# Kernel tuning notes

Hardware: AMD Instinct MI355X
Metric: run time of the kernel (lower is better)

## Reference

```python
import jax, jax.numpy as jnp
import numpy as np

IMG = 800.0
STRIDES = (4, 8, 16, 32)
SIZES = (32.0, 64.0, 128.0, 256.0)
RATIOS = (0.5, 1.0, 2.0)
A = 3
PRE_NMS_K = 1000
POST_NMS = 512
NMS_TH = 0.7
POOL = 7
_MEAN = np.array([0.485, 0.456, 0.406], np.float32).reshape(3, 1, 1)
_STD = np.array([0.229, 0.224, 0.225], np.float32).reshape(3, 1, 1)


def _conv(x, w, stride=1):
    # x: [C,H,W], w: [O,I,kh,kw]
    return jax.lax.conv_general_dilated(x[None], w, (stride, stride), 'SAME',
                                        dimension_numbers=('NCHW', 'OIHW', 'NCHW'))[0]


def _make_anchors(fh, fw, stride, size):
    cy = (np.arange(fh, dtype=np.float32) + 0.5) * stride
    cx = (np.arange(fw, dtype=np.float32) + 0.5) * stride
    ws = np.array([size / np.sqrt(r) for r in RATIOS], np.float32)
    hs = np.array([size * np.sqrt(r) for r in RATIOS], np.float32)
    gy, gx = np.meshgrid(cy, cx, indexing='ij')
    x1 = gx[..., None] - ws / 2; y1 = gy[..., None] - hs / 2
    x2 = gx[..., None] + ws / 2; y2 = gy[..., None] + hs / 2
    return jnp.asarray(np.stack([x1, y1, x2, y2], -1).reshape(-1, 4))  # [fh*fw*A,4]


def _decode(anchors, deltas):
    aw = anchors[:, 2] - anchors[:, 0]; ah = anchors[:, 3] - anchors[:, 1]
    acx = anchors[:, 0] + aw * 0.5; acy = anchors[:, 1] + ah * 0.5
    dw = jnp.clip(deltas[:, 2], -4.0, 4.0); dh = jnp.clip(deltas[:, 3], -4.0, 4.0)
    cx = acx + deltas[:, 0] * aw; cy = acy + deltas[:, 1] * ah
    w = aw * jnp.exp(dw); h = ah * jnp.exp(dh)
    boxes = jnp.stack([cx - w * 0.5, cy - h * 0.5, cx + w * 0.5, cy + h * 0.5], -1)
    return jnp.clip(boxes, 0.0, IMG)


def _nms(boxes, scores, iou_th, max_out):
    # Greedy NMS with fixed output size (jit-compatible).
    x1, y1, x2, y2 = boxes[:, 0], boxes[:, 1], boxes[:, 2], boxes[:, 3]
    areas = (x2 - x1) * (y2 - y1)

    def body(i, state):
        s, keep = state
        idx = jnp.argmax(s)
        keep = keep.at[i].set(idx)
        ix1 = jnp.maximum(x1, x1[idx]); iy1 = jnp.maximum(y1, y1[idx])
        ix2 = jnp.minimum(x2, x2[idx]); iy2 = jnp.minimum(y2, y2[idx])
        inter = jnp.maximum(ix2 - ix1, 0.0) * jnp.maximum(iy2 - iy1, 0.0)
        iou = inter / (areas + areas[idx] - inter + 1e-6)
        return jnp.where(iou > iou_th, -jnp.inf, s), keep

    _, keep = jax.lax.fori_loop(0, max_out, body, (scores, jnp.zeros(max_out, jnp.int32)))
    return keep


def _roi_align(feat, rois, scale):
    # feat: [C,H,W]; rois: [N,4] in image coords; bilinear, 1 sample per bin.
    C, H, W = feat.shape
    n = rois.shape[0]
    x1 = rois[:, 0] * scale; y1 = rois[:, 1] * scale
    bw = (rois[:, 2] - rois[:, 0]) * scale / POOL
    bh = (rois[:, 3] - rois[:, 1]) * scale / POOL
    j = jnp.arange(POOL, dtype=feat.dtype) + 0.5
    gx = jnp.broadcast_to((x1[:, None] + j * bw[:, None] - 0.5)[:, None, :], (n, POOL, POOL))
    gy = jnp.broadcast_to((y1[:, None] + j * bh[:, None] - 0.5)[:, :, None], (n, POOL, POOL))
    fx = jnp.clip(jnp.floor(gx), 0.0, W - 1); fy = jnp.clip(jnp.floor(gy), 0.0, H - 1)
    x0 = fx.astype(jnp.int32); y0 = fy.astype(jnp.int32)
    x1i = jnp.minimum(x0 + 1, W - 1); y1i = jnp.minimum(y0 + 1, H - 1)
    wx = jnp.clip(gx - fx, 0.0, 1.0); wy = jnp.clip(gy - fy, 0.0, 1.0)
    v = (feat[:, y0, x0] * (1 - wy) * (1 - wx) + feat[:, y0, x1i] * (1 - wy) * wx
         + feat[:, y1i, x0] * wy * (1 - wx) + feat[:, y1i, x1i] * wy * wx)  # [C,N,P,P]
    return jnp.transpose(v, (1, 0, 2, 3))  # [N,C,P,P]


def _forward(x, stem_w, c2_w, c3_w, c4_w, c5_w, fpn2_w, fpn3_w, fpn4_w, fpn5_w,
             rpn_w, rpn_cls_w, rpn_box_w, fc1_w, fc1_b, fc2_w, fc2_b,
             cls_w, cls_b, breg_w, breg_b):
    x = (x - _MEAN) / _STD  # ImageNet normalize
    h = jax.nn.relu(_conv(x, stem_w, 2))      # [64,400,400]
    c2 = jax.nn.relu(_conv(h, c2_w, 2))       # [256,200,200] stride 4
    c3 = jax.nn.relu(_conv(c2, c3_w, 2))      # stride 8
    c4 = jax.nn.relu(_conv(c3, c4_w, 2))      # stride 16
    c5 = jax.nn.relu(_conv(c4, c5_w, 2))      # stride 32
    feats = [_conv(c2, fpn2_w), _conv(c3, fpn3_w), _conv(c4, fpn4_w), _conv(c5, fpn5_w)]

    boxes_l, scores_l = [], []
    for lvl, f in enumerate(feats):
        t = jax.nn.relu(_conv(f, rpn_w))
        fh, fw = f.shape[1], f.shape[2]
        logits = jnp.transpose(_conv(t, rpn_cls_w), (1, 2, 0)).reshape(-1)  # [fh*fw*A]
        deltas = jnp.transpose(_conv(t, rpn_box_w).reshape(A, 4, fh, fw), (2, 3, 0, 1)).reshape(-1, 4)
        anchors = _make_anchors(fh, fw, STRIDES[lvl], SIZES[lvl])
        dec = _decode(anchors, deltas)
        k = min(PRE_NMS_K, logits.shape[0])
        sc, idx = jax.lax.top_k(logits, k)
        boxes_l.append(dec[idx]); scores_l.append(sc)

    boxes = jnp.concatenate(boxes_l, 0)
    scores = jnp.concatenate(scores_l, 0)
    keep = _nms(boxes, scores, NMS_TH, POST_NMS)
    props = boxes[keep]  # [POST_NMS,4]

    pooled = _roi_align(feats[0], props, 1.0 / STRIDES[0])  # [N,256,7,7]
    v = pooled.reshape(POST_NMS, -1)
    v = jax.nn.relu(v @ fc1_w + fc1_b)
    v = jax.nn.relu(v @ fc2_w + fc2_b)
    return v @ cls_w + cls_b, v @ breg_w + breg_b, props, scores[keep]


def setup_inputs() -> dict:
    key = jax.random.key(0)
    ks = jax.random.split(key, 18)

    def he(k, shape):
        fan_in = int(np.prod(shape[1:])) if len(shape) == 4 else shape[0]
        return jax.random.normal(k, shape, jnp.float32) * float(np.sqrt(2.0 / fan_in))

    inp = {'x': jax.random.uniform(ks[0], (3, 800, 800), jnp.float32)}
    inp['stem_w'] = he(ks[1], (64, 3, 7, 7))
    inp['c2_w'] = he(ks[2], (256, 64, 3, 3))
    for i, name in enumerate(['c3_w', 'c4_w', 'c5_w', 'fpn2_w', 'fpn3_w', 'fpn4_w', 'fpn5_w', 'rpn_w']):
        inp[name] = he(ks[3 + i], (256, 256, 3, 3))
    inp['rpn_cls_w'] = he(ks[11], (3, 256, 1, 1))
    inp['rpn_box_w'] = he(ks[12], (12, 256, 1, 1))
    inp['fc1_w'] = he(ks[13], (12544, 1024)); inp['fc1_b'] = jnp.zeros((1024,), jnp.float32)
    inp['fc2_w'] = he(ks[14], (1024, 1024)); inp['fc2_b'] = jnp.zeros((1024,), jnp.float32)
    inp['cls_w'] = he(ks[15], (1024, 2)); inp['cls_b'] = jnp.zeros((2,), jnp.float32)
    inp['breg_w'] = he(ks[16], (1024, 8)); inp['breg_b'] = jnp.zeros((8,), jnp.float32)
    return inp


def reference(x, stem_w, c2_w, c3_w, c4_w, c5_w, fpn2_w, fpn3_w, fpn4_w, fpn5_w,
              rpn_w, rpn_cls_w, rpn_box_w, fc1_w, fc1_b, fc2_w, fc2_b,
              cls_w, cls_b, breg_w, breg_b):
    return _forward(x, stem_w, c2_w, c3_w, c4_w, c5_w, fpn2_w, fpn3_w, fpn4_w, fpn5_w,
                    rpn_w, rpn_cls_w, rpn_box_w, fc1_w, fc1_b, fc2_w, fc2_b,
                    cls_w, cls_b, breg_w, breg_b)
```

## Files before the change

### kernel.cpp

```cpp
#include <hip/hip_runtime.h>
#include <math.h>


#define DI __device__ __forceinline__

typedef short short8 __attribute__((ext_vector_type(8)));
typedef float float16v __attribute__((ext_vector_type(16)));

DI unsigned fkey(float f) {
  unsigned u = __float_as_uint(f);
  return (u & 0x80000000u) ? ~u : (u | 0x80000000u);
}

DI unsigned short f2bf(float f) {
  unsigned u = __float_as_uint(f);
  unsigned r = (u + 0x7FFFu + ((u >> 16) & 1u)) >> 16;
  return (unsigned short)r;
}

__global__ __launch_bounds__(256) void stem_conv(const float* __restrict__ x,
                                                 const float* __restrict__ w,
                                                 float* __restrict__ out) {
  __shared__ float tin[3 * 37 * 37];
  __shared__ float tw[4 * 147];
  const int x0 = blockIdx.x * 16, y0 = blockIdx.y * 16, co0 = blockIdx.z * 4;
  const int tid = threadIdx.x;
  for (int i = tid; i < 4 * 147; i += 256) tw[i] = w[co0 * 147 + i];
  const int ix0 = x0 * 2 - 2, iy0 = y0 * 2 - 2;
  const float mean[3] = {0.485f, 0.456f, 0.406f};
  const float stdv[3] = {0.229f, 0.224f, 0.225f};
  for (int i = tid; i < 3 * 37 * 37; i += 256) {
    int c = i / 1369, r = i % 1369, yy = r / 37, xx = r % 37;
    int gy = iy0 + yy, gx = ix0 + xx;
    float v = 0.f;
    if ((unsigned)gy < 800u && (unsigned)gx < 800u)
      v = __fdiv_rn(__fsub_rn(x[c * 640000 + gy * 800 + gx], mean[c]), stdv[c]);
    tin[i] = v;
  }
  __syncthreads();
  const int tx = tid & 15, ty = tid >> 4;
  float acc[4] = {0.f, 0.f, 0.f, 0.f};
  for (int c = 0; c < 3; ++c)
    for (int ky = 0; ky < 7; ++ky)
#pragma unroll
      for (int kx = 0; kx < 7; ++kx) {
        float v = tin[c * 1369 + (ty * 2 + ky) * 37 + (tx * 2 + kx)];
#pragma unroll
        for (int co = 0; co < 4; ++co)
          acc[co] = fmaf(v, tw[co * 147 + c * 49 + ky * 7 + kx], acc[co]);
      }
  int ox = x0 + tx, oy = y0 + ty;
#pragma unroll
  for (int co = 0; co < 4; ++co)
    out[(size_t)(co0 + co) * 160000 + oy * 400 + ox] = fmaxf(acc[co], 0.f);
}

__global__ void repack_w32(const float* __restrict__ w,
                           float* __restrict__ wpk, int Cin) {
  int i = blockIdx.x * 256 + threadIdx.x;
  int total = 16 * Cin * 9 * 16;
  if (i >= total) return;
  int co = i & 15;
  int r = i >> 4;
  int kk = r % 9;
  int r2 = r / 9;
  int ci = r2 % Cin;
  int z = r2 / Cin;
  wpk[i] = w[((size_t)(z * 16 + co) * Cin + ci) * 9 + kk];
}

template <int CHUNK, bool RELU>
__global__ __launch_bounds__(256) void conv32_db(
    const float* __restrict__ in, const float* __restrict__ wpk,
    float* __restrict__ out, int Cin, int Hin, int Win, int Hout, int Wout) {
  constexpr int TILE = CHUNK * 612;
  constexpr int NS = (TILE + 255) / 256;
  constexpr int PADT = NS * 256;
  __shared__ __align__(16) float tin2[2][PADT];
  const int tid = threadIdx.x;
  const int tx = tid & 15, ty = tid >> 4;
  const int x0 = blockIdx.x * 32, y0 = blockIdx.y * 16;
  const int ix0 = x0 - 1, iy0 = y0 - 1;
  const size_t HWin = (size_t)Hin * Win;

  int goff[NS];
#pragma unroll
  for (int j = 0; j < NS; ++j) {
    int e = j * 256 + tid;
    int c = e / 612, r = e % 612;
    int yy = r / 34, xx = r % 34;
    int gy = iy0 + yy, gx = ix0 + xx;
    bool ok = (e < TILE) && ((unsigned)gy < (unsigned)Hin) &&
              ((unsigned)gx < (unsigned)Win);
    goff[j] = ok ? (int)((size_t)c * HWin + (size_t)gy * Win + gx) : -1;
  }

  float acc0[16], acc1[16];
#pragma unroll
  for (int co = 0; co < 16; ++co) { acc0[co] = 0.f; acc1[co] = 0.f; }

  float stg[NS];
#pragma unroll
  for (int j = 0; j < NS; ++j)
    stg[j] = (goff[j] >= 0) ? in[goff[j]] : 0.f;
#pragma unroll
  for (int j = 0; j < NS; ++j) tin2[0][j * 256 + tid] = stg[j];
  __syncthreads();

  int buf = 0;
  for (int cb = 0; cb < Cin; cb += CHUNK) {
    const bool more = (cb + CHUNK) < Cin;
    if (more) {
      const float* gsrc = in + (size_t)(cb + CHUNK) * HWin;
#pragma unroll
      for (int j = 0; j < NS; ++j)
        stg[j] = (goff[j] >= 0) ? gsrc[goff[j]] : 0.f;
    }
    for (int ci = 0; ci < CHUNK; ++ci) {
      const float4* wq = (const float4*)(wpk +
          ((size_t)blockIdx.z * Cin + (size_t)(cb + ci)) * 144);
#pragma unroll
      for (int ky = 0; ky < 3; ++ky) {
        const float* tb = &tin2[buf][ci * 612 + (ty + ky) * 34 + 2 * tx];
        float2 d0 = *(const float2*)tb;
        float2 d1 = *(const float2*)(tb + 2);
#pragma unroll
        for (int kx = 0; kx < 3; ++kx) {
          float v0 = (kx == 0) ? d0.x : (kx == 1) ? d0.y : d1.x;
          float v1 = (kx == 0) ? d0.y : (kx == 1) ? d1.x : d1.y;
          const int kk = ky * 3 + kx;
          float4 w0 = wq[kk * 4 + 0];
          float4 w1 = wq[kk * 4 + 1];
          float4 w2 = wq[kk * 4 + 2];
          float4 w3 = wq[kk * 4 + 3];
          acc0[0]  = fmaf(v0, w0.x, acc0[0]);
          acc0[1]  = fmaf(v0, w0.y, acc0[1]);
          acc0[2]  = fmaf(v0, w0.z, acc0[2]);
          acc0[3]  = fmaf(v0, w0.w, acc0[3]);
          acc1[0]  = fmaf(v1, w0.x, acc1[0]);
          acc1[1]  = fmaf(v1, w0.y, acc1[1]);
          acc1[2]  = fmaf(v1, w0.z, acc1[2]);
          acc1[3]  = fmaf(v1, w0.w, acc1[3]);
          acc0[4]  = fmaf(v0, w1.x, acc0[4]);
          acc0[5]  = fmaf(v0, w1.y, acc0[5]);
          acc0[6]  = fmaf(v0, w1.z, acc0[6]);
          acc0[7]  = fmaf(v0, w1.w, acc0[7]);
          acc1[4]  = fmaf(v1, w1.x, acc1[4]);
          acc1[5]  = fmaf(v1, w1.y, acc1[5]);
          acc1[6]  = fmaf(v1, w1.z, acc1[6]);
          acc1[7]  = fmaf(v1, w1.w, acc1[7]);
          acc0[8]  = fmaf(v0, w2.x, acc0[8]);
          acc0[9]  = fmaf(v0, w2.y, acc0[9]);
          acc0[10] = fmaf(v0, w2.z, acc0[10]);
          acc0[11] = fmaf(v0, w2.w, acc0[11]);
          acc1[8]  = fmaf(v1, w2.x, acc1[8]);
          acc1[9]  = fmaf(v1, w2.y, acc1[9]);
          acc1[10] = fmaf(v1, w2.z, acc1[10]);
          acc1[11] = fmaf(v1, w2.w, acc1[11]);
          acc0[12] = fmaf(v0, w3.x, acc0[12]);
          acc0[13] = fmaf(v0, w3.y, acc0[13]);
          acc0[14] = fmaf(v0, w3.z, acc0[14]);
          acc0[15] = fmaf(v0, w3.w, acc0[15]);
          acc1[12] = fmaf(v1, w3.x, acc1[12]);
          acc1[13] = fmaf(v1, w3.y, acc1[13]);
          acc1[14] = fmaf(v1, w3.z, acc1[14]);
          acc1[15] = fmaf(v1, w3.w, acc1[15]);
        }
      }
    }
    if (more) {
#pragma unroll
      for (int j = 0; j < NS; ++j) tin2[buf ^ 1][j * 256 + tid] = stg[j];
    }
    __syncthreads();
    buf ^= 1;
  }

  const int co0 = blockIdx.z * 16;
  int oy = y0 + ty;
  if (oy < Hout) {
    int ox = x0 + 2 * tx;
    if (ox + 1 < Wout) {
#pragma unroll
      for (int co = 0; co < 16; ++co) {
        float a = acc0[co], b = acc1[co];
        if (RELU) { a = fmaxf(a, 0.f); b = fmaxf(b, 0.f); }
        float2 st; st.x = a; st.y = b;
        *(float2*)&out[(size_t)(co0 + co) * Hout * Wout +
                       (size_t)oy * Wout + ox] = st;
      }
    } else if (ox < Wout) {
#pragma unroll
      for (int co = 0; co < 16; ++co) {
        float a = acc0[co];
        if (RELU) a = fmaxf(a, 0.f);
        out[(size_t)(co0 + co) * Hout * Wout + (size_t)oy * Wout + ox] = a;
      }
    }
  }
}

template <int CHUNK, bool RELU>
__global__ __launch_bounds__(256) void conv16_s1(const float* __restrict__ in,
                                                 const float* __restrict__ wpk,
                                                 float* __restrict__ out,
                                                 int Cin, int Hin, int Win,
                                                 int Hout, int Wout) {
  constexpr int P = 24;
  constexpr int TOT = CHUNK * 18 * 18;
  constexpr int NS = (TOT + 255) / 256;
  __shared__ __align__(16) float tin[CHUNK * 18 * P];
  const int tid = threadIdx.x;
  const int tx = tid & 15, ty = tid >> 4;
  const int x0 = blockIdx.x * 16, y0 = blockIdx.y * 16;
  const int ix0 = x0 - 1, iy0 = y0 - 1;
  const size_t HWin = (size_t)Hin * Win;

  int goff[NS], loff[NS];
#pragma unroll
  for (int j = 0; j < NS; ++j) {
    int i = tid + j * 256;
    int c = i / 324, r = i % 324;
    int yy = r / 18, xx = r % 18;
    int gy = iy0 + yy, gx = ix0 + xx;
    bool ok = (i < TOT) && ((unsigned)gy < (unsigned)Hin) &&
              ((unsigned)gx < (unsigned)Win);
    goff[j] = ok ? (int)(c * HWin + (size_t)gy * Win + gx) : -1;
    loff[j] = c * 18 * P + yy * P + xx;
  }

  float acc[16];
#pragma unroll
  for (int co = 0; co < 16; ++co) acc[co] = 0.f;

  for (int cb = 0; cb < Cin; cb += CHUNK) {
    const size_t gbase = (size_t)cb * HWin;
#pragma unroll
    for (int j = 0; j < NS; ++j) {
      int i = tid + j * 256;
      if (i < TOT) {
        float v = 0.f;
        if (goff[j] >= 0) v = in[gbase + goff[j]];
        tin[loff[j]] = v;
      }
    }
    __syncthreads();
    for (int ci = 0; ci < CHUNK; ++ci) {
      const float4* wq = (const float4*)(wpk +
          ((size_t)blockIdx.z * Cin + (size_t)(cb + ci)) * 144);
#pragma unroll
      for (int ky = 0; ky < 3; ++ky) {
#pragma unroll
        for (int kx = 0; kx < 3; ++kx) {
          const int kk = ky * 3 + kx;
          float v = tin[ci * 18 * P + (ty + ky) * P + tx + kx];
          float4 w0 = wq[kk * 4 + 0];
          float4 w1 = wq[kk * 4 + 1];
          float4 w2 = wq[kk * 4 + 2];
          float4 w3 = wq[kk * 4 + 3];
          acc[0]  = fmaf(v, w0.x, acc[0]);
          acc[1]  = fmaf(v, w0.y, acc[1]);
          acc[2]  = fmaf(v, w0.z, acc[2]);
          acc[3]  = fmaf(v, w0.w, acc[3]);
          acc[4]  = fmaf(v, w1.x, acc[4]);
          acc[5]  = fmaf(v, w1.y, acc[5]);
          acc[6]  = fmaf(v, w1.z, acc[6]);
          acc[7]  = fmaf(v, w1.w, acc[7]);
          acc[8]  = fmaf(v, w2.x, acc[8]);
          acc[9]  = fmaf(v, w2.y, acc[9]);
          acc[10] = fmaf(v, w2.z, acc[10]);
          acc[11] = fmaf(v, w2.w, acc[11]);
          acc[12] = fmaf(v, w3.x, acc[12]);
          acc[13] = fmaf(v, w3.y, acc[13]);
          acc[14] = fmaf(v, w3.z, acc[14]);
          acc[15] = fmaf(v, w3.w, acc[15]);
        }
      }
    }
    __syncthreads();
  }
  const int co0 = blockIdx.z * 16;
  int oy = y0 + ty, ox = x0 + tx;
  if (oy < Hout && ox < Wout) {
#pragma unroll
    for (int co = 0; co < 16; ++co) {
      float v = acc[co];
      if (RELU) v = fmaxf(v, 0.f);
      out[(size_t)(co0 + co) * Hout * Wout + (size_t)oy * Wout + ox] = v;
    }
  }
}

template <int CHUNK, bool RELU>
__global__ __launch_bounds__(256) void conv16_s2(const float* __restrict__ in,
                                                 const float* __restrict__ wpk,
                                                 float* __restrict__ out,
                                                 int Cin, int Hin, int Win,
                                                 int Hout, int Wout) {
  constexpr int P = 20;
  constexpr int HALF = CHUNK * 33 * P;
  constexpr int TOT = CHUNK * 33 * 33;
  constexpr int NS = (TOT + 255) / 256;
  __shared__ __align__(16) float tin2[2 * HALF];
  const int tid = threadIdx.x;
  const int tx = tid & 15, ty = tid >> 4;
  const int x0 = blockIdx.x * 16, y0 = blockIdx.y * 16;
  const int ix0 = x0 * 2, iy0 = y0 * 2;
  const size_t HWin = (size_t)Hin * Win;

  int goff[NS], loff[NS];
#pragma unroll
  for (int j = 0; j < NS; ++j) {
    int i = tid + j * 256;
    int c = i / 1089, r = i % 1089;
    int yy = r / 33, xx = r % 33;
    int gy = iy0 + yy, gx = ix0 + xx;
    bool ok = (i < TOT) && ((unsigned)gy < (unsigned)Hin) &&
              ((unsigned)gx < (unsigned)Win);
    goff[j] = ok ? (int)(c * HWin + (size_t)gy * Win + gx) : -1;
    loff[j] = c * 33 * P + yy * P + (xx >> 1) + ((xx & 1) ? HALF : 0);
  }

  float acc[16];
#pragma unroll
  for (int co = 0; co < 16; ++co) acc[co] = 0.f;

  for (int cb = 0; cb < Cin; cb += CHUNK) {
    const size_t gbase = (size_t)cb * HWin;
#pragma unroll
    for (int j = 0; j < NS; ++j) {
      int i = tid + j * 256;
      if (i < TOT) {
        float v = 0.f;
        if (goff[j] >= 0) v = in[gbase + goff[j]];
        tin2[loff[j]] = v;
      }
    }
    __syncthreads();
    for (int ci = 0; ci < CHUNK; ++ci) {
      const float4* wq = (const float4*)(wpk +
          ((size_t)blockIdx.z * Cin + (size_t)(cb + ci)) * 144);
#pragma unroll
      for (int ky = 0; ky < 3; ++ky) {
#pragma unroll
        for (int kx = 0; kx < 3; ++kx) {
          const int kk = ky * 3 + kx;
          const float* base = (kx == 1) ? (tin2 + HALF) : tin2;
          const int cadd = (kx == 2) ? 1 : 0;
          float v = base[ci * 33 * P + (2 * ty + ky) * P + tx + cadd];
          float4 w0 = wq[kk * 4 + 0];
          float4 w1 = wq[kk * 4 + 1];
          float4 w2 = wq[kk * 4 + 2];
          float4 w3 = wq[kk * 4 + 3];
          acc[0]  = fmaf(v, w0.x, acc[0]);
          acc[1]  = fmaf(v, w0.y, acc[1]);
          acc[2]  = fmaf(v, w0.z, acc[2]);
          acc[3]  = fmaf(v, w0.w, acc[3]);
          acc[4]  = fmaf(v, w1.x, acc[4]);
          acc[5]  = fmaf(v, w1.y, acc[5]);
          acc[6]  = fmaf(v, w1.z, acc[6]);
          acc[7]  = fmaf(v, w1.w, acc[7]);
          acc[8]  = fmaf(v, w2.x, acc[8]);
          acc[9]  = fmaf(v, w2.y, acc[9]);
          acc[10] = fmaf(v, w2.z, acc[10]);
          acc[11] = fmaf(v, w2.w, acc[11]);
          acc[12] = fmaf(v, w3.x, acc[12]);
          acc[13] = fmaf(v, w3.y, acc[13]);
          acc[14] = fmaf(v, w3.z, acc[14]);
          acc[15] = fmaf(v, w3.w, acc[15]);
        }
      }
    }
    __syncthreads();
  }
  const int co0 = blockIdx.z * 16;
  int oy = y0 + ty, ox = x0 + tx;
  if (oy < Hout && ox < Wout) {
#pragma unroll
    for (int co = 0; co < 16; ++co) {
      float v = acc[co];
      if (RELU) v = fmaxf(v, 0.f);
      out[(size_t)(co0 + co) * Hout * Wout + (size_t)oy * Wout + ox] = v;
    }
  }
}

__global__ __launch_bounds__(256) void transpose_t(const float* __restrict__ in,
                                                   float* __restrict__ out,
                                                   int npix) {
  __shared__ float tile[32][33];
  const int p0 = blockIdx.x * 32, c0 = blockIdx.y * 32;
  const int tx = threadIdx.x & 31, ty = threadIdx.x >> 5;
  for (int r = ty; r < 32; r += 8) {
    int p = p0 + tx;
    tile[r][tx] = (p < npix) ? in[(size_t)(c0 + r) * npix + p] : 0.f;
  }
  __syncthreads();
  for (int r = ty; r < 32; r += 8) {
    int p = p0 + r;
    if (p < npix) out[(size_t)p * 256 + c0 + tx] = tile[tx][r];
  }
}

__global__ __launch_bounds__(256) void rpn_head_decode(
    const float* __restrict__ tt, const float* __restrict__ wcls,
    const float* __restrict__ wbox, float* __restrict__ boxes,
    float* __restrict__ scores, int fh, int fw, float stride, float ws0,
    float ws1, float ws2, float hs0, float hs1, float hs2) {
  __shared__ __align__(16) float wcs[256][16];
  for (int i = threadIdx.x; i < 256 * 16; i += 256) {
    int c = i & 255, o = i >> 8;
    float v = 0.f;
    if (o < 3) v = wcls[o * 256 + c];
    else if (o < 15) v = wbox[(o - 3) * 256 + c];
    wcs[c][o] = v;
  }
  __syncthreads();
  const int npix = fh * fw;
  int p = blockIdx.x * 256 + threadIdx.x;
  if (p >= npix) return;
  float a[15];
#pragma unroll
  for (int o = 0; o < 15; ++o) a[o] = 0.f;
  const float4* tp = (const float4*)(tt + (size_t)p * 256);
#pragma unroll 4
  for (int c4 = 0; c4 < 64; ++c4) {
    float4 tv = tp[c4];
#pragma unroll
    for (int j = 0; j < 4; ++j) {
      float v = (j == 0) ? tv.x : (j == 1) ? tv.y : (j == 2) ? tv.z : tv.w;
      int c = c4 * 4 + j;
      const float4* wr = (const float4*)&wcs[c][0];
      float4 w0 = wr[0], w1 = wr[1], w2 = wr[2], w3 = wr[3];
      a[0] = fmaf(v, w0.x, a[0]);   a[1] = fmaf(v, w0.y, a[1]);
      a[2] = fmaf(v, w0.z, a[2]);   a[3] = fmaf(v, w0.w, a[3]);
      a[4] = fmaf(v, w1.x, a[4]);   a[5] = fmaf(v, w1.y, a[5]);
      a[6] = fmaf(v, w1.z, a[6]);   a[7] = fmaf(v, w1.w, a[7]);
      a[8] = fmaf(v, w2.x, a[8]);   a[9] = fmaf(v, w2.y, a[9]);
      a[10] = fmaf(v, w2.z, a[10]); a[11] = fmaf(v, w2.w, a[11]);
      a[12] = fmaf(v, w3.x, a[12]); a[13] = fmaf(v, w3.y, a[13]);
      a[14] = fmaf(v, w3.z, a[14]);
    }
  }
  const int i = p / fw, j = p % fw;
  const float acy0 = __fmul_rn((float)i + 0.5f, stride);
  const float acx0 = __fmul_rn((float)j + 0.5f, stride);
  const float WS[3] = {ws0, ws1, ws2}, HS[3] = {hs0, hs1, hs2};
#pragma unroll
  for (int an = 0; an < 3; ++an) {
    float hw = __fmul_rn(WS[an], 0.5f), hh = __fmul_rn(HS[an], 0.5f);
    float x1a = __fsub_rn(acx0, hw), x2a = __fadd_rn(acx0, hw);
    float y1a = __fsub_rn(acy0, hh), y2a = __fadd_rn(acy0, hh);
    float aw = __fsub_rn(x2a, x1a), ah = __fsub_rn(y2a, y1a);
    float acx = __fadd_rn(x1a, __fmul_rn(aw, 0.5f));
    float acy = __fadd_rn(y1a, __fmul_rn(ah, 0.5f));
    float dx = a[3 + an * 4 + 0], dy = a[3 + an * 4 + 1];
    float dw = fminf(fmaxf(a[3 + an * 4 + 2], -4.f), 4.f);
    float dh = fminf(fmaxf(a[3 + an * 4 + 3], -4.f), 4.f);
    float cx = __fadd_rn(acx, __fmul_rn(dx, aw));
    float cy = __fadd_rn(acy, __fmul_rn(dy, ah));
    float w_ = __fmul_rn(aw, expf(dw));
    float h_ = __fmul_rn(ah, expf(dh));
    int idx = p * 3 + an;
    boxes[idx * 4 + 0] =
        fminf(fmaxf(__fsub_rn(cx, __fmul_rn(w_, 0.5f)), 0.f), 800.f);
    boxes[idx * 4 + 1] =
        fminf(fmaxf(__fsub_rn(cy, __fmul_rn(h_, 0.5f)), 0.f), 800.f);
    boxes[idx * 4 + 2] =
        fminf(fmaxf(__fadd_rn(cx, __fmul_rn(w_, 0.5f)), 0.f), 800.f);
    boxes[idx * 4 + 3] =
        fminf(fmaxf(__fadd_rn(cy, __fmul_rn(h_, 0.5f)), 0.f), 800.f);
    scores[idx] = a[an];
  }
}

__global__ void hist_hi_kernel(const float* __restrict__ s, int n,
                               int* __restrict__ hist) {
  int i = blockIdx.x * blockDim.x + threadIdx.x;
  if (i < n) atomicAdd(&hist[fkey(s[i]) >> 16], 1);
}

__global__ void hist_lo_kernel(const float* __restrict__ s, int n,
                               const int* __restrict__ sel,
                               int* __restrict__ hist) {
  unsigned b = (unsigned)sel[0];
  int i = blockIdx.x * blockDim.x + threadIdx.x;
  if (i < n) {
    unsigned key = fkey(s[i]);
    if ((key >> 16) == b) atomicAdd(&hist[key & 0xffffu], 1);
  }
}

__global__ __launch_bounds__(256) void scan_hi_kernel(
    const int* __restrict__ hist, int k, int* __restrict__ sel) {
  __shared__ int csum[256];
  int t = threadIdx.x;
  int s = 0;
  for (int i = 0; i < 256; ++i) s += hist[t * 256 + i];
  csum[t] = s;
  __syncthreads();
  if (t == 0) {
    int cum = 0;
    for (int c = 255; c >= 0; --c) {
      if (cum + csum[c] >= k) {
        int cc = cum;
        for (int b = c * 256 + 255;; --b) {
          int h = hist[b];
          if (cc + h >= k) {
            sel[0] = b; sel[1] = k - cc; sel[2] = cc;
            return;
          }
          cc += h;
        }
      }
      cum += csum[c];
    }
    sel[0] = 0; sel[1] = k - cum; sel[2] = cum;
  }
}

__global__ __launch_bounds__(256) void scan_lo_kernel(
    const int* __restrict__ hist, int* __restrict__ sel) {
  __shared__ int csum[256];
  int t = threadIdx.x;
  int s = 0;
  for (int i = 0; i < 256; ++i) s += hist[t * 256 + i];
// ... 202 lines not shown
    tile[r][tx] = B[(size_t)(k0 + r) * N + n0 + tx];
  __syncthreads();
  for (int r = ty; r < 32; r += 8)
    Bt[(size_t)(n0 + r) * K + k0 + tx] = f2bf(tile[tx][r]);
}

__global__ __launch_bounds__(256) void fc_mfma(
    const unsigned short* __restrict__ A,
    const unsigned short* __restrict__ Bt,
    float* __restrict__ Cp, int M, int N, int K, int kLen) {
  const int tid = threadIdx.x;
  const int lane = tid & 63, wave = tid >> 6;
  const int n = lane & 31, half = lane >> 5;
  const int bm = blockIdx.y * 128 + wave * 32;
  const int bn = blockIdx.x * 64;
  const int k0s = blockIdx.z * kLen;
  const unsigned short* arow = A + (size_t)(bm + n) * K + half * 8;
  const unsigned short* b0row = Bt + (size_t)(bn + n) * K + half * 8;
  const unsigned short* b1row = Bt + (size_t)(bn + 32 + n) * K + half * 8;
  float16v acc0, acc1;
#pragma unroll
  for (int r = 0; r < 16; ++r) { acc0[r] = 0.f; acc1[r] = 0.f; }
  for (int k0 = k0s; k0 < k0s + kLen; k0 += 16) {
    short8 a = *(const short8*)(arow + k0);
    short8 b0 = *(const short8*)(b0row + k0);
    short8 b1 = *(const short8*)(b1row + k0);
    acc0 = __builtin_amdgcn_mfma_f32_32x32x16_bf16(a, b0, acc0, 0, 0, 0);
    acc1 = __builtin_amdgcn_mfma_f32_32x32x16_bf16(a, b1, acc1, 0, 0, 0);
  }
  float* Cz = Cp + (size_t)blockIdx.z * M * N;
#pragma unroll
  for (int r = 0; r < 16; ++r) {
    int row = bm + (r & 3) + 8 * (r >> 2) + 4 * half;
    Cz[(size_t)row * N + bn + n] = acc0[r];
    Cz[(size_t)row * N + bn + 32 + n] = acc1[r];
  }
}

__global__ void fc_combine(const float* __restrict__ p,
                           const float* __restrict__ bias,
                           float* __restrict__ out, int MN, int N, int S) {
  int i = blockIdx.x * 256 + threadIdx.x;
  if (i >= MN) return;
  float v = 0.f;
  for (int s = 0; s < S; ++s) v += p[(size_t)s * MN + i];
  out[i] = fmaxf(v + bias[i % N], 0.f);
}

__global__ __launch_bounds__(64) void heads_kernel(
    const float* __restrict__ v, const float* __restrict__ wc,
    const float* __restrict__ bc, const float* __restrict__ wb,
    const float* __restrict__ bbias, float* __restrict__ out) {
  const int m = blockIdx.x;
  const int lane = threadIdx.x;
  float acc[10];
#pragma unroll
  for (int o = 0; o < 10; ++o) acc[o] = 0.f;
  for (int k = lane; k < 1024; k += 64) {
    float x = v[(size_t)m * 1024 + k];
    acc[0] = fmaf(x, wc[k * 2 + 0], acc[0]);
    acc[1] = fmaf(x, wc[k * 2 + 1], acc[1]);
#pragma unroll
    for (int o = 0; o < 8; ++o) acc[2 + o] = fmaf(x, wb[k * 8 + o], acc[2 + o]);
  }
#pragma unroll
  for (int off = 32; off > 0; off >>= 1)
#pragma unroll
    for (int o = 0; o < 10; ++o) acc[o] += __shfl_down(acc[o], off);
  if (lane == 0) {
    out[m * 2 + 0] = acc[0] + bc[0];
    out[m * 2 + 1] = acc[1] + bc[1];
#pragma unroll
    for (int o = 0; o < 8; ++o) out[1024 + m * 8 + o] = acc[2 + o] + bbias[o];
  }
}

extern "C" void kernel_launch(void* const* d_in, const int* in_sizes, int n_in,
                              void* d_out, int out_size, void* d_ws,
                              size_t ws_size, hipStream_t stream) {
  const float* x      = (const float*)d_in[0];
  const float* w_stem = (const float*)d_in[1];
  const float* w_c2   = (const float*)d_in[2];
  const float* w_c3   = (const float*)d_in[3];
  const float* w_c4   = (const float*)d_in[4];
  const float* w_c5   = (const float*)d_in[5];
  const float* w_f2   = (const float*)d_in[6];
  const float* w_f3   = (const float*)d_in[7];
  const float* w_f4   = (const float*)d_in[8];
  const float* w_f5   = (const float*)d_in[9];
  const float* w_rpn  = (const float*)d_in[10];
  const float* w_cls  = (const float*)d_in[11];
  const float* w_box  = (const float*)d_in[12];
  const float* w_fc1  = (const float*)d_in[13];
  const float* b_fc1  = (const float*)d_in[14];
  const float* w_fc2  = (const float*)d_in[15];
  const float* b_fc2  = (const float*)d_in[16];
  const float* w_clsh = (const float*)d_in[17];
  const float* b_clsh = (const float*)d_in[18];
  const float* w_breg = (const float*)d_in[19];
  const float* b_breg = (const float*)d_in[20];
  float* dout = (float*)d_out;

  float* ws = (float*)d_ws;
  float* stem = ws;
  float* c2   = stem + 10240000;
  float* c3   = c2 + 10240000;
  float* c4   = c3 + 2560000;
  float* c5   = c4 + 640000;
  float* f2   = c5 + 160000;
  float* f3   = f2 + 10240000;
  float* f4   = f3 + 2560000;
  float* f5   = f4 + 640000;
  float* boxes_all  = f5 + 160000;
  float* scores_all = boxes_all + 16000;
  float* props      = scores_all + 4000;
  int*   hist = (int*)(props + 2048);
  int*   sel  = hist + 65536;
  float* wpkA = (float*)(sel + 16);
  float* wpkB = wpkA + 589824;
  float* wpkC = wpkB + 589824;
  float* wpkD = wpkC + 589824;
  float* wpkE = wpkD + 147456;
  float* wpkF = wpkE + 589824;
  float* wpkG = wpkF + 589824;
  float* wpkH = wpkG + 589824;
  float* wpkI = wpkH + 589824;
  float* t      = c2;
  float* tt     = stem;
  float* dec    = c3;
  float* slvl   = c4;
  int*   order  = (int*)c3;
  unsigned long long* supp =
      (unsigned long long*)(c3 + 8192);
  float* pooled = stem;
  float* fc1o   = stem + 6422528;
  float* fc2o   = fc1o + 524288;
  float* fcp    = fc2o + 524288;
  unsigned short* Abf1 = (unsigned short*)c2;
  unsigned short* Bt1  = (unsigned short*)(c2 + 3211264);
  unsigned short* Abf2 = (unsigned short*)c3;
  unsigned short* Bt2  = (unsigned short*)(c3 + 262144);

  repack_w32<<<2304, 256, 0, stream>>>(w_f2, wpkA, 256);
  repack_w32<<<2304, 256, 0, stream>>>(w_f3, wpkB, 256);
  repack_w32<<<2304, 256, 0, stream>>>(w_rpn, wpkC, 256);
  repack_w32<<<576, 256, 0, stream>>>(w_c2, wpkD, 64);
  repack_w32<<<2304, 256, 0, stream>>>(w_c3, wpkE, 256);
  repack_w32<<<2304, 256, 0, stream>>>(w_c4, wpkF, 256);
  repack_w32<<<2304, 256, 0, stream>>>(w_c5, wpkG, 256);
  repack_w32<<<2304, 256, 0, stream>>>(w_f4, wpkH, 256);
  repack_w32<<<2304, 256, 0, stream>>>(w_f5, wpkI, 256);

  stem_conv<<<dim3(25, 25, 16), 256, 0, stream>>>(x, w_stem, stem);
  conv16_s2<4, true><<<dim3(13, 13, 16), 256, 0, stream>>>(
      stem, wpkD, c2, 64, 400, 400, 200, 200);
  conv16_s2<4, true><<<dim3(7, 7, 16), 256, 0, stream>>>(
      c2, wpkE, c3, 256, 200, 200, 100, 100);
  conv16_s2<4, true><<<dim3(4, 4, 16), 256, 0, stream>>>(
      c3, wpkF, c4, 256, 100, 100, 50, 50);
  conv16_s2<4, true><<<dim3(2, 2, 16), 256, 0, stream>>>(
      c4, wpkG, c5, 256, 50, 50, 25, 25);
  conv32_db<4, false><<<dim3(7, 13, 16), 256, 0, stream>>>(
      c2, wpkA, f2, 256, 200, 200, 200, 200);
  conv32_db<4, false><<<dim3(4, 7, 16), 256, 0, stream>>>(
      c3, wpkB, f3, 256, 100, 100, 100, 100);
  conv16_s1<8, false><<<dim3(4, 4, 16), 256, 0, stream>>>(
      c4, wpkH, f4, 256, 50, 50, 50, 50);
  conv16_s1<8, false><<<dim3(2, 2, 16), 256, 0, stream>>>(
      c5, wpkI, f5, 256, 25, 25, 25, 25);

  const float* feats[4] = {f2, f3, f4, f5};
  const int dims[4] = {200, 100, 50, 25};
  const float strds[4] = {4.f, 8.f, 16.f, 32.f};
  const double szs[4] = {32.0, 64.0, 128.0, 256.0};
  for (int lvl = 0; lvl < 4; ++lvl) {
    const int d = dims[lvl];
    const int npix = d * d;
    const int N = npix * 3;
    if (lvl == 0)
      conv32_db<4, true><<<dim3(7, 13, 16), 256, 0, stream>>>(
          feats[lvl], wpkC, t, 256, d, d, d, d);
    else if (lvl == 1)
      conv32_db<4, true><<<dim3(4, 7, 16), 256, 0, stream>>>(
          feats[lvl], wpkC, t, 256, d, d, d, d);
    else if (lvl == 2)
      conv16_s1<8, true><<<dim3(4, 4, 16), 256, 0, stream>>>(
          feats[lvl], wpkC, t, 256, d, d, d, d);
    else
      conv16_s1<8, true><<<dim3(2, 2, 16), 256, 0, stream>>>(
          feats[lvl], wpkC, t, 256, d, d, d, d);
    transpose_t<<<dim3((npix + 31) / 32, 8), 256, 0, stream>>>(t, tt, npix);
    double sz = szs[lvl];
    float ws0 = (float)(sz / sqrt(0.5)), ws1 = (float)sz,
          ws2 = (float)(sz / sqrt(2.0));
    float hs0 = (float)(sz * sqrt(0.5)), hs1 = (float)sz,
          hs2 = (float)(sz * sqrt(2.0));
    rpn_head_decode<<<(npix + 255) / 256, 256, 0, stream>>>(
        tt, w_cls, w_box, dec, slvl, d, d, strds[lvl], ws0, ws1, ws2, hs0, hs1,
        hs2);
    hipMemsetAsync(hist, 0, 65536 * sizeof(int), stream);
    hist_hi_kernel<<<(N + 255) / 256, 256, 0, stream>>>(slvl, N, hist);
    scan_hi_kernel<<<1, 256, 0, stream>>>(hist, 1000, sel);
    hipMemsetAsync(hist, 0, 65536 * sizeof(int), stream);
    hist_lo_kernel<<<(N + 255) / 256, 256, 0, stream>>>(slvl, N, sel, hist);
    scan_lo_kernel<<<1, 256, 0, stream>>>(hist, sel);
    compact_kernel<<<(N + 255) / 256, 256, 0, stream>>>(
        slvl, dec, N, sel, scores_all, boxes_all, lvl * 1000);
  }

  rank_kernel<<<16, 256, 0, stream>>>(scores_all, order);
  supp_kernel<<<250, 256, 0, stream>>>(boxes_all, supp);
  nms_scan<<<1, 64, 0, stream>>>(supp, order, boxes_all, scores_all, props,
                                 dout + 5120, dout + 7168);

  roi_align_kernel<<<512, 256, 0, stream>>>(f2, props, pooled);
  cast_a<<<(6422528 + 255) / 256, 256, 0, stream>>>(pooled, Abf1, 6422528);
  cast_bt<<<dim3(32, 392), 256, 0, stream>>>(w_fc1, Bt1, 12544, 1024);
  fc_mfma<<<dim3(16, 4, 4), 256, 0, stream>>>(Abf1, Bt1, fcp, 512, 1024, 12544,
                                              3136);
  fc_combine<<<2048, 256, 0, stream>>>(fcp, b_fc1, fc1o, 524288, 1024, 4);
  cast_a<<<(524288 + 255) / 256, 256, 0, stream>>>(fc1o, Abf2, 524288);
  cast_bt<<<dim3(32, 32), 256, 0, stream>>>(w_fc2, Bt2, 1024, 1024);
  fc_mfma<<<dim3(16, 4, 4), 256, 0, stream>>>(Abf2, Bt2, fcp, 512, 1024, 1024,
                                              256);
  fc_combine<<<2048, 256, 0, stream>>>(fcp, b_fc2, fc2o, 524288, 1024, 4);
  heads_kernel<<<512, 64, 0, stream>>>(fc2o, w_clsh, b_clsh, w_breg, b_breg,
                                       dout);
}
```

Baseline: 5.303 ms.

## Restructure 3x3 conv tile to 32 output channels per block with 512 threads

The stride-1 3x3 conv kernel used for the large FPN and RPN levels now gives each of 512 threads one pixel and 32 output channels, instead of two pixels and 16 channels across 256 threads. The number of blocks along z halves, so each staged input tile is reused for twice as many output channels, which cuts global input reads and shared-memory staging per output. The costs are a 512-thread block, scalar stores in place of float2 stores, and twice as many weight loads per input value. Fewer blocks could also lower occupancy or parallelism.

```diff
diff --git a/kernel.cpp b/kernel.cpp
--- a/kernel.cpp
+++ b/kernel.cpp
@@ -69,24 +69,25 @@
   wpk[i] = w[((size_t)(z * 16 + co) * Cin + ci) * 9 + kk];
 }
 
-template <int CHUNK, bool RELU>
-__global__ __launch_bounds__(256) void conv32_db(
+template <bool RELU>
+__global__ __launch_bounds__(512) void conv32_co32(
     const float* __restrict__ in, const float* __restrict__ wpk,
     float* __restrict__ out, int Cin, int Hin, int Win, int Hout, int Wout) {
+  constexpr int CHUNK = 4;
   constexpr int TILE = CHUNK * 612;
-  constexpr int NS = (TILE + 255) / 256;
-  constexpr int PADT = NS * 256;
-  __shared__ __align__(16) float tin2[2][PADT];
+  constexpr int NS = 5;
+  __shared__ __align__(16) float tin2[2][NS * 512];
   const int tid = threadIdx.x;
-  const int tx = tid & 15, ty = tid >> 4;
+  const int tx = tid & 31, ty = tid >> 5;
   const int x0 = blockIdx.x * 32, y0 = blockIdx.y * 16;
   const int ix0 = x0 - 1, iy0 = y0 - 1;
   const size_t HWin = (size_t)Hin * Win;
+  const int zA = blockIdx.z * 2, zB = zA + 1;
 
   int goff[NS];
 #pragma unroll
   for (int j = 0; j < NS; ++j) {
-    int e = j * 256 + tid;
+    int e = j * 512 + tid;
     int c = e / 612, r = e % 612;
     int yy = r / 34, xx = r % 34;
     int gy = iy0 + yy, gx = ix0 + xx;
@@ -95,16 +96,16 @@
     goff[j] = ok ? (int)((size_t)c * HWin + (size_t)gy * Win + gx) : -1;
   }
 
-  float acc0[16], acc1[16];
-#pragma unroll
-  for (int co = 0; co < 16; ++co) { acc0[co] = 0.f; acc1[co] = 0.f; }
+  float accA[16], accB[16];
+#pragma unroll
+  for (int co = 0; co < 16; ++co) { accA[co] = 0.f; accB[co] = 0.f; }
 
   float stg[NS];
 #pragma unroll
   for (int j = 0; j < NS; ++j)
     stg[j] = (goff[j] >= 0) ? in[goff[j]] : 0.f;
 #pragma unroll
-  for (int j = 0; j < NS; ++j) tin2[0][j * 256 + tid] = stg[j];
+  for (int j = 0; j < NS; ++j) tin2[0][j * 512 + tid] = stg[j];
   __syncthreads();
 
   int buf = 0;
@@ -117,85 +118,61 @@
         stg[j] = (goff[j] >= 0) ? gsrc[goff[j]] : 0.f;
     }
     for (int ci = 0; ci < CHUNK; ++ci) {
-      const float4* wq = (const float4*)(wpk +
-          ((size_t)blockIdx.z * Cin + (size_t)(cb + ci)) * 144);
+      const float4* wqA = (const float4*)(wpk +
+          ((size_t)zA * Cin + (size_t)(cb + ci)) * 144);
+      const float4* wqB = (const float4*)(wpk +
+          ((size_t)zB * Cin + (size_t)(cb + ci)) * 144);
 #pragma unroll
       for (int ky = 0; ky < 3; ++ky) {
-        const float* tb = &tin2[buf][ci * 612 + (ty + ky) * 34 + 2 * tx];
-        float2 d0 = *(const float2*)tb;
-        float2 d1 = *(const float2*)(tb + 2);
+        const float* tb = &tin2[buf][ci * 612 + (ty + ky) * 34 + tx];
+        float c0 = tb[0];
+        float c1 = tb[1];
+        float c2v = tb[2];
 #pragma unroll
         for (int kx = 0; kx < 3; ++kx) {
-          float v0 = (kx == 0) ? d0.x : (kx == 1) ? d0.y : d1.x;
-          float v1 = (kx == 0) ? d0.y : (kx == 1) ? d1.x : d1.y;
+          float v = (kx == 0) ? c0 : (kx == 1) ? c1 : c2v;
           const int kk = ky * 3 + kx;
-          float4 w0 = wq[kk * 4 + 0];
-          float4 w1 = wq[kk * 4 + 1];
-          float4 w2 = wq[kk * 4 + 2];
-          float4 w3 = wq[kk * 4 + 3];
-          acc0[0]  = fmaf(v0, w0.x, acc0[0]);
-          acc0[1]  = fmaf(v0, w0.y, acc0[1]);
-          acc0[2]  = fmaf(v0, w0.z, acc0[2]);
-          acc0[3]  = fmaf(v0, w0.w, acc0[3]);
-          acc1[0]  = fmaf(v1, w0.x, acc1[0]);
-          acc1[1]  = fmaf(v1, w0.y, acc1[1]);
-          acc1[2]  = fmaf(v1, w0.z, acc1[2]);
-          acc1[3]  = fmaf(v1, w0.w, acc1[3]);
-          acc0[4]  = fmaf(v0, w1.x, acc0[4]);
-          acc0[5]  = fmaf(v0, w1.y, acc0[5]);
-          acc0[6]  = fmaf(v0, w1.z, acc0[6]);
-          acc0[7]  = fmaf(v0, w1.w, acc0[7]);
-          acc1[4]  = fmaf(v1, w1.x, acc1[4]);
-          acc1[5]  = fmaf(v1, w1.y, acc1[5]);
-          acc1[6]  = fmaf(v1, w1.z, acc1[6]);
-          acc1[7]  = fmaf(v1, w1.w, acc1[7]);
-          acc0[8]  = fmaf(v0, w2.x, acc0[8]);
-          acc0[9]  = fmaf(v0, w2.y, acc0[9]);
-          acc0[10] = fmaf(v0, w2.z, acc0[10]);
-          acc0[11] = fmaf(v0, w2.w, acc0[11]);
-          acc1[8]  = fmaf(v1, w2.x, acc1[8]);
-          acc1[9]  = fmaf(v1, w2.y, acc1[9]);
-          acc1[10] = fmaf(v1, w2.z, acc1[10]);
-          acc1[11] = fmaf(v1, w2.w, acc1[11]);
-          acc0[12] = fmaf(v0, w3.x, acc0[12]);
-          acc0[13] = fmaf(v0, w3.y, acc0[13]);
-          acc0[14] = fmaf(v0, w3.z, acc0[14]);
-          acc0[15] = fmaf(v0, w3.w, acc0[15]);
-          acc1[12] = fmaf(v1, w3.x, acc1[12]);
-          acc1[13] = fmaf(v1, w3.y, acc1[13]);
-          acc1[14] = fmaf(v1, w3.z, acc1[14]);
-          acc1[15] = fmaf(v1, w3.w, acc1[15]);
+#pragma unroll
+          for (int g = 0; g < 4; ++g) {
+            float4 w = wqA[kk * 4 + g];
+            accA[g * 4 + 0] = fmaf(v, w.x, accA[g * 4 + 0]);
+            accA[g * 4 + 1] = fmaf(v, w.y, accA[g * 4 + 1]);
+            accA[g * 4 + 2] = fmaf(v, w.z, accA[g * 4 + 2]);
+            accA[g * 4 + 3] = fmaf(v, w.w, accA[g * 4 + 3]);
+          }
+#pragma unroll
+          for (int g = 0; g < 4; ++g) {
+            float4 w = wqB[kk * 4 + g];
+            accB[g * 4 + 0] = fmaf(v, w.x, accB[g * 4 + 0]);
+            accB[g * 4 + 1] = fmaf(v, w.y, accB[g * 4 + 1]);
+            accB[g * 4 + 2] = fmaf(v, w.z, accB[g * 4 + 2]);
+            accB[g * 4 + 3] = fmaf(v, w.w, accB[g * 4 + 3]);
+          }
         }
       }
     }
     if (more) {
 #pragma unroll
-      for (int j = 0; j < NS; ++j) tin2[buf ^ 1][j * 256 + tid] = stg[j];
+      for (int j = 0; j < NS; ++j) tin2[buf ^ 1][j * 512 + tid] = stg[j];
     }
     __syncthreads();
     buf ^= 1;
   }
 
-  const int co0 = blockIdx.z * 16;
-  int oy = y0 + ty;
-  if (oy < Hout) {
-    int ox = x0 + 2 * tx;
-    if (ox + 1 < Wout) {
-#pragma unroll
-      for (int co = 0; co < 16; ++co) {
-        float a = acc0[co], b = acc1[co];
-        if (RELU) { a = fmaxf(a, 0.f); b = fmaxf(b, 0.f); }
-        float2 st; st.x = a; st.y = b;
-        *(float2*)&out[(size_t)(co0 + co) * Hout * Wout +
-                       (size_t)oy * Wout + ox] = st;
-      }
-    } else if (ox < Wout) {
-#pragma unroll
-      for (int co = 0; co < 16; ++co) {
-        float a = acc0[co];
-        if (RELU) a = fmaxf(a, 0.f);
-        out[(size_t)(co0 + co) * Hout * Wout + (size_t)oy * Wout + ox] = a;
-      }
+  const int co0 = blockIdx.z * 32;
+  int oy = y0 + ty, ox = x0 + tx;
+  if (oy < Hout && ox < Wout) {
+#pragma unroll
+    for (int co = 0; co < 16; ++co) {
+      float a = accA[co];
+      if (RELU) a = fmaxf(a, 0.f);
+      out[(size_t)(co0 + co) * Hout * Wout + (size_t)oy * Wout + ox] = a;
+    }
+#pragma unroll
+    for (int co = 0; co < 16; ++co) {
+      float a = accB[co];
+      if (RELU) a = fmaxf(a, 0.f);
+      out[(size_t)(co0 + 16 + co) * Hout * Wout + (size_t)oy * Wout + ox] = a;
     }
   }
 }
@@ -888,9 +865,9 @@
       c3, wpkF, c4, 256, 100, 100, 50, 50);
   conv16_s2<4, true><<<dim3(2, 2, 16), 256, 0, stream>>>(
       c4, wpkG, c5, 256, 50, 50, 25, 25);
-  conv32_db<4, false><<<dim3(7, 13, 16), 256, 0, stream>>>(
+  conv32_co32<false><<<dim3(7, 13, 8), 512, 0, stream>>>(
       c2, wpkA, f2, 256, 200, 200, 200, 200);
-  conv32_db<4, false><<<dim3(4, 7, 16), 256, 0, stream>>>(
+  conv32_co32<false><<<dim3(4, 7, 8), 512, 0, stream>>>(
       c3, wpkB, f3, 256, 100, 100, 100, 100);
   conv16_s1<8, false><<<dim3(4, 4, 16), 256, 0, stream>>>(
       c4, wpkH, f4, 256, 50, 50, 50, 50);
@@ -906,10 +883,10 @@
     const int npix = d * d;
     const int N = npix * 3;
     if (lvl == 0)
-      conv32_db<4, true><<<dim3(7, 13, 16), 256, 0, stream>>>(
+      conv32_co32<true><<<dim3(7, 13, 8), 512, 0, stream>>>(
           feats[lvl], wpkC, t, 256, d, d, d, d);
     else if (lvl == 1)
-      conv32_db<4, true><<<dim3(4, 7, 16), 256, 0, stream>>>(
+      conv32_co32<true><<<dim3(4, 7, 8), 512, 0, stream>>>(
           feats[lvl], wpkC, t, 256, d, d, d, d);
     else if (lvl == 2)
       conv16_s1<8, true><<<dim3(4, 4, 16), 256, 0, stream>>>(
```

Measured after the change: 5.901 ms. +11.3%, slower.

## Double-buffer input tiles in conv16 stride-1 and stride-2 kernels

Applied to the files above, without the earlier changes.

Converts the conv16_s1 and conv16_s2 kernels into double-buffered versions. Each thread loads the next channel chunk from global memory into registers while computing on the current shared tile, then writes it to the alternate buffer, so each chunk needs one barrier instead of two. Chunk sizes are halved (8→4, 4→2) so the doubled shared-memory footprint stays about the same. In exchange the kernels use more registers for staging and run more loop iterations.

```diff
diff --git a/kernel.cpp b/kernel.cpp
--- a/kernel.cpp
+++ b/kernel.cpp
@@ -201,15 +201,13 @@
 }
 
 template <int CHUNK, bool RELU>
-__global__ __launch_bounds__(256) void conv16_s1(const float* __restrict__ in,
-                                                 const float* __restrict__ wpk,
-                                                 float* __restrict__ out,
-                                                 int Cin, int Hin, int Win,
-                                                 int Hout, int Wout) {
+__global__ __launch_bounds__(256) void conv16_s1_db(
+    const float* __restrict__ in, const float* __restrict__ wpk,
+    float* __restrict__ out, int Cin, int Hin, int Win, int Hout, int Wout) {
   constexpr int P = 24;
   constexpr int TOT = CHUNK * 18 * 18;
   constexpr int NS = (TOT + 255) / 256;
-  __shared__ __align__(16) float tin[CHUNK * 18 * P];
+  __shared__ __align__(16) float tin2[2][CHUNK * 18 * P];
   const int tid = threadIdx.x;
   const int tx = tid & 15, ty = tid >> 4;
   const int x0 = blockIdx.x * 16, y0 = blockIdx.y * 16;
@@ -226,25 +224,31 @@
     bool ok = (i < TOT) && ((unsigned)gy < (unsigned)Hin) &&
               ((unsigned)gx < (unsigned)Win);
     goff[j] = ok ? (int)(c * HWin + (size_t)gy * Win + gx) : -1;
-    loff[j] = c * 18 * P + yy * P + xx;
+    loff[j] = (i < TOT) ? (c * 18 * P + yy * P + xx) : 0;
   }
 
   float acc[16];
 #pragma unroll
   for (int co = 0; co < 16; ++co) acc[co] = 0.f;
 
+  float stg[NS];
+#pragma unroll
+  for (int j = 0; j < NS; ++j)
+    stg[j] = (goff[j] >= 0) ? in[goff[j]] : 0.f;
+#pragma unroll
+  for (int j = 0; j < NS; ++j)
+    if (tid + j * 256 < TOT) tin2[0][loff[j]] = stg[j];
+  __syncthreads();
+
+  int buf = 0;
   for (int cb = 0; cb < Cin; cb += CHUNK) {
-    const size_t gbase = (size_t)cb * HWin;
-#pragma unroll
-    for (int j = 0; j < NS; ++j) {
-      int i = tid + j * 256;
-      if (i < TOT) {
-        float v = 0.f;
-        if (goff[j] >= 0) v = in[gbase + goff[j]];
-        tin[loff[j]] = v;
-      }
-    }
-    __syncthreads();
+    const bool more = (cb + CHUNK) < Cin;
+    if (more) {
+      const float* gsrc = in + (size_t)(cb + CHUNK) * HWin;
+#pragma unroll
+      for (int j = 0; j < NS; ++j)
+        stg[j] = (goff[j] >= 0) ? gsrc[goff[j]] : 0.f;
+    }
     for (int ci = 0; ci < CHUNK; ++ci) {
       const float4* wq = (const float4*)(wpk +
           ((size_t)blockIdx.z * Cin + (size_t)(cb + ci)) * 144);
@@ -253,7 +257,7 @@
 #pragma unroll
         for (int kx = 0; kx < 3; ++kx) {
           const int kk = ky * 3 + kx;
-          float v = tin[ci * 18 * P + (ty + ky) * P + tx + kx];
+          float v = tin2[buf][ci * 18 * P + (ty + ky) * P + tx + kx];
           float4 w0 = wq[kk * 4 + 0];
           float4 w1 = wq[kk * 4 + 1];
           float4 w2 = wq[kk * 4 + 2];
@@ -277,7 +281,13 @@
         }
       }
     }
+    if (more) {
+#pragma unroll
+      for (int j = 0; j < NS; ++j)
+        if (tid + j * 256 < TOT) tin2[buf ^ 1][loff[j]] = stg[j];
+    }
     __syncthreads();
+    buf ^= 1;
   }
   const int co0 = blockIdx.z * 16;
   int oy = y0 + ty, ox = x0 + tx;
@@ -292,16 +302,14 @@
 }
 
 template <int CHUNK, bool RELU>
-__global__ __launch_bounds__(256) void conv16_s2(const float* __restrict__ in,
-                                                 const float* __restrict__ wpk,
-                                                 float* __restrict__ out,
-                                                 int Cin, int Hin, int Win,
-                                                 int Hout, int Wout) {
+__global__ __launch_bounds__(256) void conv16_s2_db(
+    const float* __restrict__ in, const float* __restrict__ wpk,
+    float* __restrict__ out, int Cin, int Hin, int Win, int Hout, int Wout) {
   constexpr int P = 20;
   constexpr int HALF = CHUNK * 33 * P;
   constexpr int TOT = CHUNK * 33 * 33;
   constexpr int NS = (TOT + 255) / 256;
-  __shared__ __align__(16) float tin2[2 * HALF];
+  __shared__ __align__(16) float tin2[2][2 * HALF];
   const int tid = threadIdx.x;
   const int tx = tid & 15, ty = tid >> 4;
   const int x0 = blockIdx.x * 16, y0 = blockIdx.y * 16;
@@ -318,25 +326,33 @@
     bool ok = (i < TOT) && ((unsigned)gy < (unsigned)Hin) &&
               ((unsigned)gx < (unsigned)Win);
     goff[j] = ok ? (int)(c * HWin + (size_t)gy * Win + gx) : -1;
-    loff[j] = c * 33 * P + yy * P + (xx >> 1) + ((xx & 1) ? HALF : 0);
+    loff[j] = (i < TOT)
+                  ? (c * 33 * P + yy * P + (xx >> 1) + ((xx & 1) ? HALF : 0))
+                  : 0;
   }
 
   float acc[16];
 #pragma unroll
   for (int co = 0; co < 16; ++co) acc[co] = 0.f;
 
+  float stg[NS];
+#pragma unroll
+  for (int j = 0; j < NS; ++j)
+    stg[j] = (goff[j] >= 0) ? in[goff[j]] : 0.f;
+#pragma unroll
+  for (int j = 0; j < NS; ++j)
+    if (tid + j * 256 < TOT) tin2[0][loff[j]] = stg[j];
+  __syncthreads();
+
+  int buf = 0;
   for (int cb = 0; cb < Cin; cb += CHUNK) {
-    const size_t gbase = (size_t)cb * HWin;
-#pragma unroll
-    for (int j = 0; j < NS; ++j) {
-      int i = tid + j * 256;
-      if (i < TOT) {
-        float v = 0.f;
-        if (goff[j] >= 0) v = in[gbase + goff[j]];
-        tin2[loff[j]] = v;
-      }
-    }
-    __syncthreads();
+    const bool more = (cb + CHUNK) < Cin;
+    if (more) {
+      const float* gsrc = in + (size_t)(cb + CHUNK) * HWin;
+#pragma unroll
+      for (int j = 0; j < NS; ++j)
+        stg[j] = (goff[j] >= 0) ? gsrc[goff[j]] : 0.f;
+    }
     for (int ci = 0; ci < CHUNK; ++ci) {
       const float4* wq = (const float4*)(wpk +
           ((size_t)blockIdx.z * Cin + (size_t)(cb + ci)) * 144);
@@ -345,7 +361,8 @@
 #pragma unroll
         for (int kx = 0; kx < 3; ++kx) {
           const int kk = ky * 3 + kx;
-          const float* base = (kx == 1) ? (tin2 + HALF) : tin2;
+          const float* base = (kx == 1) ? (&tin2[buf][0] + HALF)
+                                        : &tin2[buf][0];
           const int cadd = (kx == 2) ? 1 : 0;
           float v = base[ci * 33 * P + (2 * ty + ky) * P + tx + cadd];
           float4 w0 = wq[kk * 4 + 0];
@@ -371,7 +388,13 @@
         }
       }
     }
+    if (more) {
+#pragma unroll
+      for (int j = 0; j < NS; ++j)
+        if (tid + j * 256 < TOT) tin2[buf ^ 1][loff[j]] = stg[j];
+    }
     __syncthreads();
+    buf ^= 1;
   }
   const int co0 = blockIdx.z * 16;
   int oy = y0 + ty, ox = x0 + tx;
@@ -880,21 +903,21 @@
   repack_w32<<<2304, 256, 0, stream>>>(w_f5, wpkI, 256);
 
   stem_conv<<<dim3(25, 25, 16), 256, 0, stream>>>(x, w_stem, stem);
-  conv16_s2<4, true><<<dim3(13, 13, 16), 256, 0, stream>>>(
+  conv16_s2_db<2, true><<<dim3(13, 13, 16), 256, 0, stream>>>(
       stem, wpkD, c2, 64, 400, 400, 200, 200);
-  conv16_s2<4, true><<<dim3(7, 7, 16), 256, 0, stream>>>(
+  conv16_s2_db<2, true><<<dim3(7, 7, 16), 256, 0, stream>>>(
       c2, wpkE, c3, 256, 200, 200, 100, 100);
-  conv16_s2<4, true><<<dim3(4, 4, 16), 256, 0, stream>>>(
+  conv16_s2_db<2, true><<<dim3(4, 4, 16), 256, 0, stream>>>(
       c3, wpkF, c4, 256, 100, 100, 50, 50);
-  conv16_s2<4, true><<<dim3(2, 2, 16), 256, 0, stream>>>(
+  conv16_s2_db<2, true><<<dim3(2, 2, 16), 256, 0, stream>>>(
       c4, wpkG, c5, 256, 50, 50, 25, 25);
   conv32_db<4, false><<<dim3(7, 13, 16), 256, 0, stream>>>(
       c2, wpkA, f2, 256, 200, 200, 200, 200);
   conv32_db<4, false><<<dim3(4, 7, 16), 256, 0, stream>>>(
       c3, wpkB, f3, 256, 100, 100, 100, 100);
-  conv16_s1<8, false><<<dim3(4, 4, 16), 256, 0, stream>>>(
+  conv16_s1_db<4, false><<<dim3(4, 4, 16), 256, 0, stream>>>(
       c4, wpkH, f4, 256, 50, 50, 50, 50);
-  conv16_s1<8, false><<<dim3(2, 2, 16), 256, 0, stream>>>(
+  conv16_s1_db<4, false><<<dim3(2, 2, 16), 256, 0, stream>>>(
       c5, wpkI, f5, 256, 25, 25, 25, 25);
 
   const float* feats[4] = {f2, f3, f4, f5};
@@ -912,10 +935,10 @@
       conv32_db<4, true><<<dim3(4, 7, 16), 256, 0, stream>>>(
           feats[lvl], wpkC, t, 256, d, d, d, d);
     else if (lvl == 2)
-      conv16_s1<8, true><<<dim3(4, 4, 16), 256, 0, stream>>>(
+      conv16_s1_db<4, true><<<dim3(4, 4, 16), 256, 0, stream>>>(
           feats[lvl], wpkC, t, 256, d, d, d, d);
     else
-      conv16_s1<8, true><<<dim3(2, 2, 16), 256, 0, stream>>>(
+      conv16_s1_db<4, true><<<dim3(2, 2, 16), 256, 0, stream>>>(
           feats[lvl], wpkC, t, 256, d, d, d, d);
     transpose_t<<<dim3((npix + 31) / 32, 8), 256, 0, stream>>>(t, tt, npix);
     double sz = szs[lvl];
```

Result: slower. 6.173 ms (+16.4%).
